# Kernel tuning notes

Measured on AMD Instinct MI355X. Metric: run time of the kernel, lower is better.

## Reference

```python
import jax, jax.numpy as jnp
import numpy as np

B, S, D = 8, 2048, 512

def setup_inputs() -> dict:
    key = jax.random.key(0)
    ks = jax.random.split(key, 9)
    scale = 1.0 / np.sqrt(D)
    return {
        "x": jax.random.normal(ks[0], (B, S, D), dtype=jnp.float32),
        "attention_mask": jax.random.uniform(ks[1], (B, S), dtype=jnp.float32),
        "Wq": jax.random.normal(ks[2], (D, D), dtype=jnp.float32) * scale,
        "bq": jax.random.normal(ks[3], (D,), dtype=jnp.float32) * 0.01,
        "Wk": jax.random.normal(ks[4], (D, D), dtype=jnp.float32) * scale,
        "bk": jax.random.normal(ks[5], (D,), dtype=jnp.float32) * 0.01,
        "Wv": jax.random.normal(ks[6], (D, D), dtype=jnp.float32) * scale,
        "bv": jax.random.normal(ks[7], (D,), dtype=jnp.float32) * 0.01,
    }

def reference(x, attention_mask, Wq, bq, Wk, bk, Wv, bv):
    # Single-head self-attention, full O(S^2) scores as in the original.
    q = jnp.einsum('bsd,df->bsf', x, Wq) + bq  # [B,S,D]
    k = jnp.einsum('bsd,df->bsf', x, Wk) + bk
    v = jnp.einsum('bsd,df->bsf', x, Wv) + bv
    scores = jnp.einsum('bqd,bkd->bqk', q, k) / jnp.sqrt(jnp.float32(D))  # [B,S,S]
    attn = jax.nn.softmax(scores, axis=2)
    weighted = jnp.einsum('bqk,bkd->bqd', attn, v)  # [B,S,D]
    # mask applied multiplicatively to the output, per original code
    return weighted * attention_mask[:, :, None]
```

## Files before the change

kernel.cpp:

```cpp
#include <hip/hip_runtime.h>
#include <math.h>
#include <stdint.h>


typedef _Float16 f16x8 __attribute__((ext_vector_type(8)));
typedef _Float16 f16x4 __attribute__((ext_vector_type(4)));
typedef _Float16 f16x2 __attribute__((ext_vector_type(2)));
typedef float f32x4 __attribute__((ext_vector_type(4)));

__device__ __forceinline__ void async16(const _Float16* g, _Float16* l) {
    __builtin_amdgcn_global_load_lds(
        (const __attribute__((address_space(1))) unsigned int*)(uintptr_t)g,
        (__attribute__((address_space(3))) unsigned int*)(unsigned int)(uintptr_t)l,
        16, 0, 0);
}

__device__ __forceinline__ float frag_sum8(f16x8 v, float acc) {
#if __has_builtin(__builtin_amdgcn_fdot2)
    const f16x2 one2 = {(_Float16)1.f, (_Float16)1.f};
    const f16x2* p = (const f16x2*)&v;
    acc = __builtin_amdgcn_fdot2(p[0], one2, acc, false);
    acc = __builtin_amdgcn_fdot2(p[1], one2, acc, false);
    acc = __builtin_amdgcn_fdot2(p[2], one2, acc, false);
    acc = __builtin_amdgcn_fdot2(p[3], one2, acc, false);
#else
#pragma unroll
    for (int j = 0; j < 8; j++) acc += (float)v[j];
#endif
    return acc;
}

template <bool WITH_RS>
__device__ __forceinline__ void mfma_gemm_core64(
    const _Float16* __restrict__ A, int lda,
    const _Float16* __restrict__ B, int ldb,
    int K, int row0, int col0,
    _Float16* As, _Float16* Bs, f32x4 acc[4][4], float rs[4])
{
    const int tid  = threadIdx.x;
    const int lane = tid & 63;
    const int wave = tid >> 6;
    const int wm   = wave >> 1, wn = wave & 1;

    const int rc  = lane >> 3;
    const int swz = ((lane & 7) ^ rc) * 8;

    const _Float16* gA[4]; const _Float16* gB[4];
    _Float16* lA[4]; _Float16* lB[4];
#pragma unroll
    for (int i = 0; i < 4; i++) {
        int c = wave * 4 + i;
        gA[i] = A + (size_t)(row0 + 8 * c + rc) * lda + swz;
        gB[i] = B + (size_t)(col0 + 8 * c + rc) * ldb + swz;
        lA[i] = As + c * 512;
        lB[i] = Bs + c * 512;
    }

    const int fr = lane & 15;
    const int q  = lane >> 4;
    const int fx = fr & 7;

    for (int k0 = 0; k0 < K; k0 += 64) {
        __syncthreads();
#pragma unroll
        for (int i = 0; i < 4; i++) {
            async16(gA[i] + k0, lA[i]);
            async16(gB[i] + k0, lB[i]);
        }
        __syncthreads();
#pragma unroll
        for (int step = 0; step < 2; step++) {
            f16x8 af[4], bf[4];
#pragma unroll
            for (int t = 0; t < 4; t++) {
                int ra = wm * 64 + t * 16 + fr;
                int rb = wn * 64 + t * 16 + fr;
                int kc = ((step * 4 + q) ^ fx) * 8;
                af[t] = *(const f16x8*)&As[ra * 64 + kc];
                bf[t] = *(const f16x8*)&Bs[rb * 64 + kc];
            }
            if (WITH_RS) {
#pragma unroll
                for (int t = 0; t < 4; t++) rs[t] = frag_sum8(af[t], rs[t]);
            }
#pragma unroll
            for (int tm = 0; tm < 4; tm++)
#pragma unroll
                for (int tn = 0; tn < 4; tn++)
                    acc[tm][tn] = __builtin_amdgcn_mfma_f32_16x16x32_f16(
                        af[tm], bf[tn], acc[tm][tn], 0, 0, 0);
        }
    }
}

__global__ __launch_bounds__(256) void prep(
    const float* __restrict__ x,
    const float* __restrict__ Wq, const float* __restrict__ Wk,
    const float* __restrict__ Wv,
    _Float16* __restrict__ Xh,
    _Float16* __restrict__ WqT, _Float16* __restrict__ WkT,
    _Float16* __restrict__ WvT)
{
    const int bid = blockIdx.x;
    if (bid < 8192) {
        int i = (bid * 256 + threadIdx.x) * 4;
        float4 v = *(const float4*)(x + i);
        f16x4 h;
        h.x = (_Float16)v.x; h.y = (_Float16)v.y;
        h.z = (_Float16)v.z; h.w = (_Float16)v.w;
        *(f16x4*)&Xh[i] = h;
    } else {
        int t = bid - 8192;
        int z = t >> 10;
        const float* W = (z == 0) ? Wq : (z == 1) ? Wk : Wv;
        _Float16* Wt   = (z == 0) ? WqT : (z == 1) ? WkT : WvT;
        int idx = (t & 1023) * 256 + threadIdx.x;
        int n = idx >> 9, k = idx & 511;
        Wt[idx] = (_Float16)W[k * 512 + n];
    }
}

__global__ __launch_bounds__(256) void proj_mfma(
    const _Float16* __restrict__ Xh,
    const _Float16* __restrict__ WqT, const float* __restrict__ bq,
    const _Float16* __restrict__ WkT, const float* __restrict__ bk,
    const _Float16* __restrict__ WvT, const float* __restrict__ bv,
    _Float16* __restrict__ Qh, _Float16* __restrict__ Kh,
    _Float16* __restrict__ Vt)
{
    __shared__ __align__(16) _Float16 smem[2 * 128 * 64];
    _Float16* As = smem;
    _Float16* Bs = smem + 128 * 64;

    const int z = blockIdx.z;
    f32x4 acc[4][4];
#pragma unroll
    for (int i = 0; i < 4; i++)
#pragma unroll
        for (int j = 0; j < 4; j++) acc[i][j] = (f32x4){0.f, 0.f, 0.f, 0.f};
    float rs_unused[4];

    const int lane = threadIdx.x & 63, wave = threadIdx.x >> 6;
    const int wm = wave >> 1, wn = wave & 1;
    const int er = (lane >> 4) * 4, ec = lane & 15;

    if (z < 2) {
        const _Float16* Wt = (z == 0) ? WqT : WkT;
        const float* bias  = (z == 0) ? bq : bk;
        _Float16* P        = (z == 0) ? Qh : Kh;
        const float sc     = (z == 0) ? 0.04419417382415922f : 1.0f;
        const int row0 = blockIdx.x * 128, col0 = blockIdx.y * 128;
        mfma_gemm_core64<false>(Xh, 512, Wt, 512, 512, row0, col0, As, Bs, acc,
                                rs_unused);
#pragma unroll
        for (int tm = 0; tm < 4; tm++)
#pragma unroll
            for (int tn = 0; tn < 4; tn++) {
                int col = col0 + wn * 64 + tn * 16 + ec;
                float bb = bias[col];
#pragma unroll
                for (int r = 0; r < 4; r++) {
                    int row = row0 + wm * 64 + tm * 16 + er + r;
                    P[(size_t)row * 512 + col] = (_Float16)((acc[tm][tn][r] + bb) * sc);
                }
            }
    } else {
        const int row0 = blockIdx.y * 128;
        const int col0 = blockIdx.x * 128;
        mfma_gemm_core64<false>(WvT, 512, Xh, 512, 512, row0, col0, As, Bs, acc,
                                rs_unused);
#pragma unroll
        for (int tm = 0; tm < 4; tm++)
#pragma unroll
            for (int tn = 0; tn < 4; tn++) {
                int col = col0 + wn * 64 + tn * 16 + ec;
                size_t obase = (size_t)(col >> 11) * (512 * 2048) + (col & 2047);
#pragma unroll
                for (int r = 0; r < 4; r++) {
                    int row = row0 + wm * 64 + tm * 16 + er + r;
                    Vt[obase + (size_t)row * 2048] = (_Float16)(acc[tm][tn][r] + bv[row]);
                }
            }
    }
}

__global__ __launch_bounds__(256) void scores_mfma(
    const _Float16* __restrict__ Qh, const _Float16* __restrict__ Kh,
    _Float16* __restrict__ Sh)
{
    __shared__ __align__(16) _Float16 smem[2 * 128 * 64];
    _Float16* As = smem;
    _Float16* Bs = smem + 128 * 64;
    const int bid = blockIdx.x;
    const int b   = bid & 7;
    const int rem = bid >> 3;
    const int col0 = (rem & 15) * 128;
    const int row0 = (rem >> 4) * 128;

    const _Float16* A = Qh + (size_t)b * 2048 * 512;
    const _Float16* B = Kh + (size_t)b * 2048 * 512;
    _Float16* S = Sh + (size_t)b * 2048 * 2048;

    f32x4 acc[4][4];
#pragma unroll
    for (int i = 0; i < 4; i++)
#pragma unroll
        for (int j = 0; j < 4; j++) acc[i][j] = (f32x4){0.f, 0.f, 0.f, 0.f};
    float rs_unused[4];

    mfma_gemm_core64<false>(A, 512, B, 512, 512, row0, col0, As, Bs, acc,
                            rs_unused);

    const int lane = threadIdx.x & 63, wave = threadIdx.x >> 6;
    const int wm = wave >> 1, wn = wave & 1;
    const int er = (lane >> 4) * 4, ec = lane & 15;
#pragma unroll
    for (int tm = 0; tm < 4; tm++)
#pragma unroll
        for (int tn = 0; tn < 4; tn++) {
            int col = col0 + wn * 64 + tn * 16 + ec;
#pragma unroll
            for (int r = 0; r < 4; r++) {
                int row = row0 + wm * 64 + tm * 16 + er + r;
                S[(size_t)row * 2048 + col] = (_Float16)__expf(acc[tm][tn][r]);
            }
        }
}

__global__ __launch_bounds__(256) void av_mfma(
    const _Float16* __restrict__ Sh, const _Float16* __restrict__ Vt,
    const float* __restrict__ mask, float* __restrict__ out)
{
    __shared__ __align__(16) _Float16 smem[2 * 128 * 64];
    __shared__ float l_s[128];
    _Float16* As = smem;
    _Float16* Bs = smem + 128 * 64;
    const int bid = blockIdx.x;
    const int b   = bid & 7;
    const int rem = bid >> 3;
    const int col0 = (rem & 3) * 128;
    const int row0 = (rem >> 2) * 128;

    const _Float16* A = Sh + (size_t)b * 2048 * 2048;
    const _Float16* B = Vt + (size_t)b * 512 * 2048;
    float* O = out + (size_t)b * 2048 * 512;
    const float* mk = mask + (size_t)b * 2048;

    f32x4 acc[4][4];
#pragma unroll
    for (int i = 0; i < 4; i++)
#pragma unroll
        for (int j = 0; j < 4; j++) acc[i][j] = (f32x4){0.f, 0.f, 0.f, 0.f};
    float rs[4] = {0.f, 0.f, 0.f, 0.f};

    mfma_gemm_core64<true>(A, 2048, B, 2048, 2048, row0, col0, As, Bs, acc, rs);

    const int lane = threadIdx.x & 63, wave = threadIdx.x >> 6;
    const int wm = wave >> 1, wn = wave & 1;
    const int er = (lane >> 4) * 4, ec = lane & 15;

#pragma unroll
    for (int t = 0; t < 4; t++) {
        rs[t] += __shfl_xor(rs[t], 16, 64);
        rs[t] += __shfl_xor(rs[t], 32, 64);
    }
    if (wn == 0 && lane < 16) {
#pragma unroll
        for (int t = 0; t < 4; t++) l_s[wm * 64 + t * 16 + lane] = rs[t];
    }
    __syncthreads();

#pragma unroll
    for (int tm = 0; tm < 4; tm++)
#pragma unroll
        for (int r = 0; r < 4; r++) {
            int lrow = wm * 64 + tm * 16 + er + r;
            int row = row0 + lrow;
            float s = mk[row] / l_s[lrow];
#pragma unroll
            for (int tn = 0; tn < 4; tn++) {
                int col = col0 + wn * 64 + tn * 16 + ec;
                O[(size_t)row * 512 + col] = acc[tm][tn][r] * s;
            }
        }
}

extern "C" void kernel_launch(void* const* d_in, const int* in_sizes, int n_in,
                              void* d_out, int out_size, void* d_ws, size_t ws_size,
                              hipStream_t stream) {
    const float* x    = (const float*)d_in[0];
    const float* mask = (const float*)d_in[1];
    const float* Wq   = (const float*)d_in[2];
    const float* bq   = (const float*)d_in[3];
    const float* Wk   = (const float*)d_in[4];
    const float* bk   = (const float*)d_in[5];
    const float* Wv   = (const float*)d_in[6];
    const float* bv   = (const float*)d_in[7];
    float* out = (float*)d_out;

    const size_t BSD = (size_t)8 * 2048 * 512;
    _Float16* base = (_Float16*)d_ws;
    _Float16* Qh  = base;
    _Float16* Kh  = Qh + BSD;
    _Float16* Vt  = Kh + BSD;
    _Float16* WqT = Vt + BSD;
    _Float16* WkT = WqT + 512 * 512;
    _Float16* WvT = WkT + 512 * 512;
    _Float16* Xh  = WvT + 512 * 512;
    _Float16* Sh  = Xh;

    dim3 blk(256);
    prep<<<dim3(8192 + 3 * 1024), blk, 0, stream>>>(
        x, Wq, Wk, Wv, Xh, WqT, WkT, WvT);
    proj_mfma<<<dim3(128, 4, 3), blk, 0, stream>>>(
        Xh, WqT, bq, WkT, bk, WvT, bv, Qh, Kh, Vt);
    scores_mfma<<<dim3(2048), blk, 0, stream>>>(Qh, Kh, Sh);
    av_mfma<<<dim3(512), blk, 0, stream>>>(Sh, Vt, mask, out);
}
```

Measured before the change: 226.3 us.

## Double-buffer LDS tiles in MFMA GEMM core with prefetch of next K-slice

Replaces the shared GEMM core with a double-buffered version that uses 32-wide K slices. The async global-to-LDS loads for the next slice are issued before the MFMAs on the current one, so memory latency can overlap compute, and each step needs one barrier instead of two. The LDS swizzle and load mapping are redone for the 32-element rows. Total LDS stays the same. In exchange, each barrier now covers half as much MFMA work, and the loop depends on the barrier also waiting for the outstanding async loads.

```diff
diff --git a/kernel.cpp b/kernel.cpp
--- a/kernel.cpp
+++ b/kernel.cpp
@@ -31,65 +31,67 @@
 }
 
 template <bool WITH_RS>
-__device__ __forceinline__ void mfma_gemm_core64(
+__device__ __forceinline__ void mfma_gemm_dbuf(
     const _Float16* __restrict__ A, int lda,
     const _Float16* __restrict__ B, int ldb,
     int K, int row0, int col0,
-    _Float16* As, _Float16* Bs, f32x4 acc[4][4], float rs[4])
+    _Float16* sm, f32x4 acc[4][4], float rs[4])
 {
     const int tid  = threadIdx.x;
     const int lane = tid & 63;
     const int wave = tid >> 6;
     const int wm   = wave >> 1, wn = wave & 1;
 
-    const int rc  = lane >> 3;
-    const int swz = ((lane & 7) ^ rc) * 8;
-
-    const _Float16* gA[4]; const _Float16* gB[4];
-    _Float16* lA[4]; _Float16* lB[4];
-#pragma unroll
-    for (int i = 0; i < 4; i++) {
-        int c = wave * 4 + i;
-        gA[i] = A + (size_t)(row0 + 8 * c + rc) * lda + swz;
-        gB[i] = B + (size_t)(col0 + 8 * c + rc) * ldb + swz;
-        lA[i] = As + c * 512;
-        lB[i] = Bs + c * 512;
-    }
+    const int rL  = lane >> 2;
+    const int key = ((lane >> 2) ^ (lane >> 4)) & 3;
+    const int cs  = ((lane & 3) ^ key) * 8;
+
+    const _Float16* gA0 = A + (size_t)(row0 + wave * 32      + rL) * lda + cs;
+    const _Float16* gA1 = A + (size_t)(row0 + wave * 32 + 16 + rL) * lda + cs;
+    const _Float16* gB0 = B + (size_t)(col0 + wave * 32      + rL) * ldb + cs;
+    const _Float16* gB1 = B + (size_t)(col0 + wave * 32 + 16 + rL) * ldb + cs;
 
     const int fr = lane & 15;
     const int q  = lane >> 4;
-    const int fx = fr & 7;
-
-    for (int k0 = 0; k0 < K; k0 += 64) {
+    const int kc = ((q ^ ((fr ^ (fr >> 2)) & 3))) * 8;
+
+    const int S = K >> 5;
+
+    async16(gA0, sm +        wave * 1024);
+    async16(gA1, sm +        wave * 1024 + 512);
+    async16(gB0, sm + 4096 + wave * 1024);
+    async16(gB1, sm + 4096 + wave * 1024 + 512);
+
+#pragma unroll 2
+    for (int s = 0; s < S; s++) {
         __syncthreads();
-#pragma unroll
-        for (int i = 0; i < 4; i++) {
-            async16(gA[i] + k0, lA[i]);
-            async16(gB[i] + k0, lB[i]);
-        }
-        __syncthreads();
-#pragma unroll
-        for (int step = 0; step < 2; step++) {
-            f16x8 af[4], bf[4];
-#pragma unroll
-            for (int t = 0; t < 4; t++) {
-                int ra = wm * 64 + t * 16 + fr;
-                int rb = wn * 64 + t * 16 + fr;
-                int kc = ((step * 4 + q) ^ fx) * 8;
-                af[t] = *(const f16x8*)&As[ra * 64 + kc];
-                bf[t] = *(const f16x8*)&Bs[rb * 64 + kc];
-            }
-            if (WITH_RS) {
-#pragma unroll
-                for (int t = 0; t < 4; t++) rs[t] = frag_sum8(af[t], rs[t]);
-            }
-#pragma unroll
-            for (int tm = 0; tm < 4; tm++)
-#pragma unroll
-                for (int tn = 0; tn < 4; tn++)
-                    acc[tm][tn] = __builtin_amdgcn_mfma_f32_16x16x32_f16(
-                        af[tm], bf[tn], acc[tm][tn], 0, 0, 0);
-        }
+        if (s + 1 < S) {
+            int k = (s + 1) << 5;
+            _Float16* dA = sm + ((s + 1) & 1) * 8192;
+            _Float16* dB = dA + 4096;
+            async16(gA0 + k, dA + wave * 1024);
+            async16(gA1 + k, dA + wave * 1024 + 512);
+            async16(gB0 + k, dB + wave * 1024);
+            async16(gB1 + k, dB + wave * 1024 + 512);
+        }
+        const _Float16* As = sm + (s & 1) * 8192;
+        const _Float16* Bs = As + 4096;
+        f16x8 af[4], bf[4];
+#pragma unroll
+        for (int t = 0; t < 4; t++) {
+            af[t] = *(const f16x8*)&As[(wm * 64 + t * 16 + fr) * 32 + kc];
+            bf[t] = *(const f16x8*)&Bs[(wn * 64 + t * 16 + fr) * 32 + kc];
+        }
+        if (WITH_RS) {
+#pragma unroll
+            for (int t = 0; t < 4; t++) rs[t] = frag_sum8(af[t], rs[t]);
+        }
+#pragma unroll
+        for (int tm = 0; tm < 4; tm++)
+#pragma unroll
+            for (int tn = 0; tn < 4; tn++)
+                acc[tm][tn] = __builtin_amdgcn_mfma_f32_16x16x32_f16(
+                    af[tm], bf[tn], acc[tm][tn], 0, 0, 0);
     }
 }
 
@@ -128,9 +130,7 @@
     _Float16* __restrict__ Qh, _Float16* __restrict__ Kh,
     _Float16* __restrict__ Vt)
 {
-    __shared__ __align__(16) _Float16 smem[2 * 128 * 64];
-    _Float16* As = smem;
-    _Float16* Bs = smem + 128 * 64;
+    __shared__ __align__(16) _Float16 smem[16384];
 
     const int z = blockIdx.z;
     f32x4 acc[4][4];
@@ -150,8 +150,8 @@
         _Float16* P        = (z == 0) ? Qh : Kh;
         const float sc     = (z == 0) ? 0.04419417382415922f : 1.0f;
         const int row0 = blockIdx.x * 128, col0 = blockIdx.y * 128;
-        mfma_gemm_core64<false>(Xh, 512, Wt, 512, 512, row0, col0, As, Bs, acc,
-                                rs_unused);
+        mfma_gemm_dbuf<false>(Xh, 512, Wt, 512, 512, row0, col0, smem, acc,
+                              rs_unused);
 #pragma unroll
         for (int tm = 0; tm < 4; tm++)
 #pragma unroll
@@ -167,8 +167,8 @@
     } else {
         const int row0 = blockIdx.y * 128;
         const int col0 = blockIdx.x * 128;
-        mfma_gemm_core64<false>(WvT, 512, Xh, 512, 512, row0, col0, As, Bs, acc,
-                                rs_unused);
+        mfma_gemm_dbuf<false>(WvT, 512, Xh, 512, 512, row0, col0, smem, acc,
+                              rs_unused);
 #pragma unroll
         for (int tm = 0; tm < 4; tm++)
 #pragma unroll
@@ -188,9 +188,7 @@
     const _Float16* __restrict__ Qh, const _Float16* __restrict__ Kh,
     _Float16* __restrict__ Sh)
 {
-    __shared__ __align__(16) _Float16 smem[2 * 128 * 64];
-    _Float16* As = smem;
-    _Float16* Bs = smem + 128 * 64;
+    __shared__ __align__(16) _Float16 smem[16384];
     const int bid = blockIdx.x;
     const int b   = bid & 7;
     const int rem = bid >> 3;
@@ -208,8 +206,8 @@
         for (int j = 0; j < 4; j++) acc[i][j] = (f32x4){0.f, 0.f, 0.f, 0.f};
     float rs_unused[4];
 
-    mfma_gemm_core64<false>(A, 512, B, 512, 512, row0, col0, As, Bs, acc,
-                            rs_unused);
+    mfma_gemm_dbuf<false>(A, 512, B, 512, 512, row0, col0, smem, acc,
+                          rs_unused);
 
     const int lane = threadIdx.x & 63, wave = threadIdx.x >> 6;
     const int wm = wave >> 1, wn = wave & 1;
@@ -231,10 +229,8 @@
     const _Float16* __restrict__ Sh, const _Float16* __restrict__ Vt,
     const float* __restrict__ mask, float* __restrict__ out)
 {
-    __shared__ __align__(16) _Float16 smem[2 * 128 * 64];
+    __shared__ __align__(16) _Float16 smem[16384];
     __shared__ float l_s[128];
-    _Float16* As = smem;
-    _Float16* Bs = smem + 128 * 64;
     const int bid = blockIdx.x;
     const int b   = bid & 7;
     const int rem = bid >> 3;
@@ -253,7 +249,7 @@
         for (int j = 0; j < 4; j++) acc[i][j] = (f32x4){0.f, 0.f, 0.f, 0.f};
     float rs[4] = {0.f, 0.f, 0.f, 0.f};
 
-    mfma_gemm_core64<true>(A, 2048, B, 2048, 2048, row0, col0, As, Bs, acc, rs);
+    mfma_gemm_dbuf<true>(A, 2048, B, 2048, 2048, row0, col0, smem, acc, rs);
 
     const int lane = threadIdx.x & 63, wave = threadIdx.x >> 6;
     const int wm = wave >> 1, wn = wave & 1;
```

Measured after the change: 239.6 us. +5.9%, slower.
